# Kernel tuning notes

Measured on AMD Instinct MI355X. Metric: run time of the kernel, lower is better.

Reference implementation:

```python
import jax, jax.numpy as jnp
import numpy as np

T, B, DG, DH, S = 24, 128, 256, 512, 3
LAM, ETA, EPS_A = 0.95, 0.5, 1e-6   # lambda_decay, eta, epsilon (A-update)
LN_EPS = 1e-5                        # torch LayerNorm default eps
EPS_N = 1e-6                         # norm clamp in inner loop


def setup_inputs() -> dict:
    key = jax.random.key(0)
    ks = jax.random.split(key, 3)
    return {
        "z_seq": jax.random.normal(ks[0], (T, B, DG), jnp.float32),
        "W_h": jax.random.normal(ks[1], (DH, DH), jnp.float32) * (2.0 / DH) ** 0.5,  # kaiming-ish
        "W_g": jax.random.normal(ks[2], (DH, DG), jnp.float32) * (1.0 / DG) ** 0.5,  # xavier-ish
        "b_h": jnp.zeros((DH,), jnp.float32),
        "gamma": jnp.ones((DH,), jnp.float32),
        "beta": jnp.zeros((DH,), jnp.float32),
        "alpha_fw": jnp.ones((1,), jnp.float32),
    }


def _layernorm(x, g, b):
    m = jnp.mean(x, -1, keepdims=True)
    v = jnp.mean((x - m) ** 2, -1, keepdims=True)
    return (x - m) * jax.lax.rsqrt(v + LN_EPS) * g + b


def _compute_k(a):
    k_pos = 1.0 + jax.nn.softplus(a)
    k_neg = 1.0 / (1.0 + jax.nn.softplus(-a))
    return jnp.where(a >= 0, k_pos, k_neg)


def reference(z_seq, W_h, W_g, b_h, gamma, beta, alpha_fw):
    k = _compute_k(alpha_fw[0])

    def step(carry, inp):
        h, A = carry            # h: [B, DH], A: [B, DH, DH]
        z_t, upd = inp          # z_t: [B, DG], upd: scalar bool (t < T-1)
        h_base = h @ W_h.T + z_t @ W_g.T + b_h
        h_s = jax.nn.relu(h_base)
        for _ in range(S):      # inner associative-memory iteration
            Ah = jnp.einsum('bij,bj->bi', A, h_s)
            dot = jnp.sum(h_s * Ah, -1, keepdims=True)
            n1 = jnp.maximum(jnp.linalg.norm(h_s, axis=-1, keepdims=True), EPS_N)
            n2 = jnp.maximum(jnp.linalg.norm(Ah, axis=-1, keepdims=True), EPS_N)
            R_pos = jnp.clip(dot / (n1 * n2), 0.0, 1.0)
            alpha_dyn = 1.0 - (1.0 - R_pos) ** k
            h_s = jax.nn.relu(_layernorm((1.0 - alpha_dyn ** 2) * h_base + alpha_dyn * Ah, gamma, beta))
        # fast-weight Hebbian update (skipped at the last timestep)
        hn2 = jnp.sum(h_s ** 2, -1, keepdims=True) + EPS_A            # [B, 1]
        delta = h_s[:, :, None] * h_s[:, None, :] / hn2[:, :, None]   # [B, DH, DH]
        A_new = jnp.where(upd, LAM * A + ETA * delta, A)
        return (h_s, A_new), None

    h0 = jnp.zeros((B, DH), z_seq.dtype)
    A0 = jnp.zeros((B, DH, DH), z_seq.dtype)
    upd = jnp.arange(T) < (T - 1)
    (h, A), _ = jax.lax.scan(step, (h0, A0), (z_seq, upd))
    return h
```

## Files before the change

### kernel.cpp

```cpp
#include <hip/hip_runtime.h>
#include <hip/hip_fp16.h>
#include <math.h>

#define T_STEPS 24
#define BATCH   128
#define DGI     256
#define DHI     512
#define S_ITERS 3
#define LAMBDA  0.95f
#define ETA     0.5f
#define EPS_A   1e-6f
#define LN_EPS  1e-5f
#define EPS_N   1e-6f
#define HIST_MAX 23
#define NG4      6

static __device__ __forceinline__ float dot2(unsigned int a, unsigned int b, float c) {
#if __has_builtin(__builtin_amdgcn_fdot2)
    typedef _Float16 h2v __attribute__((ext_vector_type(2)));
    return __builtin_amdgcn_fdot2(__builtin_bit_cast(h2v, a),
                                  __builtin_bit_cast(h2v, b), c, false);
#else
    const __half2 ha = __builtin_bit_cast(__half2, a);
    const __half2 hb = __builtin_bit_cast(__half2, b);
    const float2 fa = __half22float2(ha);
    const float2 fb = __half22float2(hb);
    return fmaf(fa.x, fb.x, fmaf(fa.y, fb.y, c));
#endif
}

static __device__ __forceinline__ unsigned int rdlane_u(unsigned int v, int l) {
#if __has_builtin(__builtin_amdgcn_readlane)
    return __builtin_amdgcn_readlane(v, l);
#else
    return __shfl((int)v, l, 64);
#endif
}
static __device__ __forceinline__ float rdlane_f(float v, int l) {
    return __uint_as_float(rdlane_u(__float_as_uint(v), l));
}

static __device__ __forceinline__ float wsum(float v) {
    #pragma unroll
    for (int off = 32; off > 0; off >>= 1) v += __shfl_xor(v, off, 64);
    return v;
}
static __device__ __forceinline__ float dot8(float4 a, float4 b, float4 c, float4 d) {
    float r = a.x * c.x;
    r = fmaf(a.y, c.y, r); r = fmaf(a.z, c.z, r); r = fmaf(a.w, c.w, r);
    r = fmaf(b.x, d.x, r); r = fmaf(b.y, d.y, r); r = fmaf(b.z, d.z, r);
    r = fmaf(b.w, d.w, r);
    return r;
}
static __device__ __forceinline__ float sum8(float4 a, float4 b) {
    return ((a.x + a.y) + (a.z + a.w)) + ((b.x + b.y) + (b.z + b.w));
}

__global__ void transpose_k(const float* __restrict__ src, float* __restrict__ dst,
                            int R, int C) {
    __shared__ float tile[32][33];
    const int tx = threadIdx.x & 31;
    const int ty = threadIdx.x >> 5;
    const int c0 = blockIdx.x * 32;
    const int r0 = blockIdx.y * 32;
    #pragma unroll
    for (int i = 0; i < 32; i += 8)
        tile[ty + i][tx] = src[(size_t)(r0 + ty + i) * C + (c0 + tx)];
    __syncthreads();
    #pragma unroll
    for (int i = 0; i < 32; i += 8)
        dst[(size_t)(c0 + ty + i) * R + (r0 + tx)] = tile[tx][ty + i];
}

__global__ __launch_bounds__(512)
void pack_wh_k(const float* __restrict__ Wh, unsigned int* __restrict__ P) {
    const int j2 = blockIdx.x;
    const int i  = threadIdx.x;
    const float2 w = *(const float2*)(Wh + (size_t)i * DHI + 2 * j2);
    const __half2 h = __floats2half2_rn(w.x, w.y);
    P[(size_t)j2 * DHI + i] = __builtin_bit_cast(unsigned int, h);
}

__global__ __launch_bounds__(512)
void zproj_k(const float* __restrict__ z_seq, const float* __restrict__ WgT,
             float* __restrict__ zp) {
    __shared__ __align__(16) float  sh_z[8][DGI];
    __shared__ __align__(16) float4 sh_acc[8][4][128];
    const int b    = blockIdx.x;
    const int t0   = blockIdx.y * 8;
    const int tid  = threadIdx.x;
    const int lane = tid & 63;
    const int wave = tid >> 6;
    {
        const float4* src =
            (const float4*)(z_seq + ((size_t)(t0 + wave) * BATCH + b) * DGI);
        ((float4*)sh_z[wave])[lane] = src[lane];
    }
    __syncthreads();

    const int i4  = tid & 127;
    const int jg  = tid >> 7;
    const int jlo = jg * 64;
    float zreg[8];
    #pragma unroll
    for (int tt = 0; tt < 8; ++tt) zreg[tt] = sh_z[tt][jlo + lane];

    float4 acc[8];
    #pragma unroll
    for (int tt = 0; tt < 8; ++tt) acc[tt] = make_float4(0.f, 0.f, 0.f, 0.f);

    const float4* w4 = (const float4*)WgT;
    #pragma unroll 4
    for (int jj = 0; jj < 64; ++jj) {
        const float4 wv = w4[(size_t)(jlo + jj) * 128 + i4];
        #pragma unroll
        for (int tt = 0; tt < 8; ++tt) {
            const float zv = rdlane_f(zreg[tt], jj);
            acc[tt].x = fmaf(wv.x, zv, acc[tt].x);
            acc[tt].y = fmaf(wv.y, zv, acc[tt].y);
            acc[tt].z = fmaf(wv.z, zv, acc[tt].z);
            acc[tt].w = fmaf(wv.w, zv, acc[tt].w);
        }
    }
    #pragma unroll
    for (int tt = 0; tt < 8; ++tt) sh_acc[tt][jg][i4] = acc[tt];
    __syncthreads();

    const float* af = (const float*)sh_acc;
    #pragma unroll
    for (int tt = 0; tt < 8; ++tt) {
        const int o = tt * 4 * 512;
        const float v = (af[o + tid] + af[o + 512 + tid]) +
                        (af[o + 1024 + tid] + af[o + 1536 + tid]);
        zp[((size_t)b * T_STEPS + t0 + tt) * DHI + tid] = v;
    }
}

__global__ __launch_bounds__(512)
void rnn_v3(const float* __restrict__ zp,
            const unsigned int* __restrict__ P,
            const float* __restrict__ b_h,
            const float* __restrict__ gamma,
            const float* __restrict__ beta,
            const float* __restrict__ alpha_fw,
            float* __restrict__ out) {
    __shared__ __align__(16) float  sh_hist[HIST_MAX][DHI];
    __shared__ __align__(16) float4 sh_hT4[NG4][DHI];
    __shared__ __align__(16) float4 sh_G4[NG4][64];
    __shared__ __align__(16) float  sh_hs[2][DHI];
    __shared__ __align__(16) float  sh_hb[DHI];
    __shared__ __align__(16) float4 sh_part[4][128];
    __shared__ __align__(16) unsigned int sh_h2[DHI / 2];
    __shared__ __align__(16) float  sh_coef[32];
    __shared__ __align__(16) float  sh_dot[32];
    __shared__ __align__(16) float  sh_dhb[32];
    __shared__ __align__(16) float  sh_rsum[32];
    __shared__ float sh_misc[2];

    const int tid  = threadIdx.x;
    const int lane = tid & 63;
    const int wave = tid >> 6;
    const int b    = blockIdx.x;

    const float bh_r = b_h[tid];
    const float g_r  = gamma[tid];
    const float bt_r = beta[tid];

    float kpow;
    {
        const float a  = alpha_fw[0];
        const float ax = fabsf(a);
        const float sp = (ax > 20.f) ? ax : log1pf(expf(ax));
        kpow = (a >= 0.f) ? (1.f + sp) : (1.f / (1.f + sp));
    }

    {
        const float4 z4 = make_float4(0.f, 0.f, 0.f, 0.f);
        for (int i = tid; i < NG4 * DHI; i += DHI) ((float4*)sh_hT4)[i] = z4;
        if (tid < NG4 * 64) ((float4*)sh_G4)[tid] = z4;
        if (tid < 32) { sh_coef[tid] = 0.f; sh_dot[tid] = 0.f;
                        sh_dhb[tid]  = 0.f; sh_rsum[tid] = 0.f; }
        if (tid < 2) sh_misc[tid] = 0.f;
    }
    __syncthreads();

    int   p = 0;
    float hs_i = 0.f, hbase_i = 0.f;
    const size_t zbase = (size_t)b * T_STEPS * DHI + tid;
    float zv = zp[zbase];

    for (int t = 0; t < T_STEPS; ++t) {
        if (t > 0) {
            const int i4 = tid & 127;
            const int jg = tid >> 7;
            const uint4* __restrict__ wp = (const uint4*)P;
            const unsigned int hreg = sh_h2[(jg << 6) | lane];
            const int base = (jg << 6) * 128 + i4;
            float4 acc = make_float4(0.f, 0.f, 0.f, 0.f);
            #pragma unroll 8
            for (int jj = 0; jj < 64; ++jj) {
                const unsigned int hh = rdlane_u(hreg, jj);
                const uint4 wv = wp[base + jj * 128];
                acc.x = dot2(wv.x, hh, acc.x);
                acc.y = dot2(wv.y, hh, acc.y);
                acc.z = dot2(wv.z, hh, acc.z);
                acc.w = dot2(wv.w, hh, acc.w);
            }
            sh_part[jg][i4] = acc;
            __syncthreads();
            const float* pp = (const float*)sh_part;
            hbase_i = bh_r + zv +
                      ((pp[tid] + pp[512 + tid]) + (pp[1024 + tid] + pp[1536 + tid]));
        } else {
            hbase_i = bh_r + zv;
        }
        sh_hb[tid] = hbase_i;
        hs_i = fmaxf(hbase_i, 0.f);
        p ^= 1;
        sh_hs[p][tid] = hs_i;
        __syncthreads();

        if (t + 1 < T_STEPS) zv = zp[zbase + (size_t)(t + 1) * DHI];

        const int niter = (t == 0) ? 1 : S_ITERS;
        for (int it = 0; it < niter; ++it) {
            {
                const float4* h4p = (const float4*)sh_hs[p];
                const float4 ha = h4p[lane], hc = h4p[64 + lane];
                float4 ba, bc;
                if (it == 0) {
                    const float4* b4p = (const float4*)sh_hb;
                    ba = b4p[lane]; bc = b4p[64 + lane];
                }
                for (int s = wave; s <= t; s += 8) {
                    if (s == t) {
                        float d = dot8(ha, hc, ha, hc);
                        if (it == 0) {
                            float s1 = sum8(ba, bc);
                            float s2 = dot8(ba, bc, ba, bc);
                            d = wsum(d); s1 = wsum(s1); s2 = wsum(s2);
                            if (lane == 0) { sh_dot[t] = d;
                                             sh_misc[0] = s1; sh_misc[1] = s2; }
                        } else {
                            d = wsum(d);
                            if (lane == 0) sh_dot[t] = d;
                        }
                    } else {
                        const float4* v4 = (const float4*)sh_hist[s];
                        const float4 va = v4[lane], vc = v4[64 + lane];
                        float d = dot8(va, vc, ha, hc);
                        if (it == 0) {
                            float e = dot8(va, vc, ba, bc);
                            d = wsum(d); e = wsum(e);
                            if (lane == 0) { sh_dot[s] = d; sh_dhb[s] = e; }
                        } else {
                            d = wsum(d);
                            if (lane == 0) sh_dot[s] = d;
                        }
                    }
                }
            }
            __syncthreads();

            float pa = 0.f, SA = 0.f, SHA = 0.f, gsum = 0.f, Ah = 0.f;
            {
                const float4* c4 = (const float4*)sh_coef;
                const float4* d4 = (const float4*)sh_dot;
                const float4* e4 = (const float4*)sh_dhb;
                const float4* r4 = (const float4*)sh_rsum;
                const int ng = (t + 4) >> 2;
                for (int g = 0; g < ng; ++g) {
                    const float4 cc = c4[g], dd = d4[g], ee = e4[g], rr = r4[g];
                    const float4 gg = sh_G4[g][lane];
                    const float4 hv = sh_hT4[g][tid];
                    const float w0 = cc.x * dd.x, w1 = cc.y * dd.y;
                    const float w2 = cc.z * dd.z, w3 = cc.w * dd.w;
                    pa   = fmaf(w0, dd.x, fmaf(w1, dd.y, fmaf(w2, dd.z, fmaf(w3, dd.w, pa))));
                    SA   = fmaf(w0, rr.x, fmaf(w1, rr.y, fmaf(w2, rr.z, fmaf(w3, rr.w, SA))));
                    SHA  = fmaf(w0, ee.x, fmaf(w1, ee.y, fmaf(w2, ee.z, fmaf(w3, ee.w, SHA))));
                    gsum = fmaf(w0, gg.x, fmaf(w1, gg.y, fmaf(w2, gg.z, fmaf(w3, gg.w, gsum))));
                    Ah   = fmaf(w0, hv.x, fmaf(w1, hv.y, fmaf(w2, hv.z, fmaf(w3, hv.w, Ah))));
                }
            }
            const float wl = (lane < 32) ? sh_coef[lane] * sh_dot[lane] : 0.f;
            const float pb = wsum(wl * gsum);

            const float n1 = fmaxf(sqrtf(sh_dot[t]), EPS_N);
            const float n2 = fmaxf(sqrtf(fmaxf(pb, 0.f)), EPS_N);
            float R = pa / (n1 * n2);
            R = fminf(fmaxf(R, 0.f), 1.f);
            const float alpha = 1.f - __powf(1.f - R, kpow);
            const float c = 1.f - alpha * alpha;

            const float S1 = sh_misc[0], S2 = sh_misc[1];
            const float mean = (c * S1 + alpha * SA) * (1.f / DHI);
            float var = (c * c * S2 + 2.f * c * alpha * SHA + alpha * alpha * pb)
                        * (1.f / DHI) - mean * mean;
            var = fmaxf(var, 0.f);
            const float rstd = rsqrtf(var + LN_EPS);

            const float y = fmaf(c, hbase_i, alpha * Ah);
            hs_i = fmaxf(fmaf((y - mean) * rstd, g_r, bt_r), 0.f);
            p ^= 1;
            sh_hs[p][tid] = hs_i;
            if (it == niter - 1 && t + 1 < T_STEPS) {
                const float partner = __shfl_xor(hs_i, 1);
                if (!(tid & 1)) {
                    const __half2 h2 = __floats2half2_rn(hs_i, partner);
                    sh_h2[tid >> 1] = __builtin_bit_cast(unsigned int, h2);
                }
            }
            __syncthreads();
        }

        if (t < T_STEPS - 1) {
            const float4* h4p = (const float4*)sh_hs[p];
            const float4 ha = h4p[lane], hc = h4p[64 + lane];
            for (int s = wave; s <= t; s += 8) {
                if (s == t) {
                    float d  = dot8(ha, hc, ha, hc);
                    float rs = sum8(ha, hc);
                    d = wsum(d); rs = wsum(rs);
                    if (lane == 0) {
                        ((float*)&sh_G4[t >> 2][t])[t & 3] = d;
                        sh_coef[t] = ETA / (d + EPS_A);
                        sh_rsum[t] = rs;
                    }
                } else {
                    const float4* v4 = (const float4*)sh_hist[s];
                    const float4 va = v4[lane], vc = v4[64 + lane];
                    float d = dot8(va, vc, ha, hc);
                    d = wsum(d);
                    if (lane == 0) {
                        ((float*)&sh_G4[t >> 2][s])[t & 3] = d;
                        ((float*)&sh_G4[s >> 2][t])[s & 3] = d;
                    }
                }
            }
            if (tid < t) sh_coef[tid] *= LAMBDA;
            sh_hist[t][tid] = hs_i;
            ((float*)&sh_hT4[t >> 2][tid])[t & 3] = hs_i;
        } else {
            out[(size_t)b * DHI + tid] = hs_i;
        }
    }
}

__global__ __launch_bounds__(512)
void corernn_fb(const float* __restrict__ z_seq, const float* __restrict__ Wh,
                const float* __restrict__ Wg, const float* __restrict__ b_h,
                const float* __restrict__ gamma, const float* __restrict__ beta,
                const float* __restrict__ alpha_fw, float* __restrict__ out) {
    __shared__ __align__(16) float sh_hist[HIST_MAX][DHI];
    __shared__ __align__(16) float sh_hs[2][DHI];
    __shared__ __align__(16) float sh_G[HIST_MAX][64];
    __shared__ float  sh_coef[32];
    __shared__ float  sh_dot[32];
    __shared__ float2 sh_red[8];
    __shared__ __align__(16) float sh_z[DGI];

    const int tid  = threadIdx.x;
    const int lane = tid & 63;
    const int wave = tid >> 6;
    const int b    = blockIdx.x;
    const float bh_r = b_h[tid];
    const float g_r  = gamma[tid];
    const float bt_r = beta[tid];
    float kpow;
    {
        const float a  = alpha_fw[0];
        const float ax = fabsf(a);
        const float sp = (ax > 20.f) ? ax : log1pf(expf(ax));
        kpow = (a >= 0.f) ? (1.f + sp) : (1.f / (1.f + sp));
    }
    for (int i = tid; i < HIST_MAX * 64; i += DHI) ((float*)sh_G)[i] = 0.f;
    if (tid < DGI) sh_z[tid] = z_seq[(size_t)b * DGI + tid];
    __syncthreads();

    int p = 0;
    float hs_i = 0.f, hbase_i = 0.f;
    for (int t = 0; t < T_STEPS; ++t) {
        float a0 = bh_r, a1 = 0.f, a2 = 0.f, a3 = 0.f;
        {
            const float4* wrow = (const float4*)(Wg + (size_t)tid * DGI);
            const float4* z4   = (const float4*)sh_z;
            #pragma unroll 4
            for (int j4 = 0; j4 < DGI / 4; ++j4) {
                const float4 w = wrow[j4]; const float4 h = z4[j4];
                a0 = fmaf(w.x, h.x, a0); a1 = fmaf(w.y, h.y, a1);
                a2 = fmaf(w.z, h.z, a2); a3 = fmaf(w.w, h.w, a3);
            }
        }
        if (t > 0) {
            const float4* wrow = (const float4*)(Wh + (size_t)tid * DHI);
            const float4* h4   = (const float4*)sh_hs[p];
            #pragma unroll 4
            for (int j4 = 0; j4 < DHI / 4; ++j4) {
                const float4 w = wrow[j4]; const float4 h = h4[j4];
                a0 = fmaf(w.x, h.x, a0); a1 = fmaf(w.y, h.y, a1);
                a2 = fmaf(w.z, h.z, a2); a3 = fmaf(w.w, h.w, a3);
            }
        }
        hbase_i = (a0 + a1) + (a2 + a3);
        hs_i = fmaxf(hbase_i, 0.f);
        p ^= 1; sh_hs[p][tid] = hs_i;
        __syncthreads();

        const int niter = (t == 0) ? 1 : S_ITERS;
        for (int it = 0; it < niter; ++it) {
            const float* hcur = sh_hs[p];
            float h8[8];
            #pragma unroll
            for (int q = 0; q < 8; ++q) h8[q] = hcur[lane + 64 * q];
            for (int s = wave; s <= t; s += 8) {
                float d = 0.f;
                if (s == t) {
                    #pragma unroll
                    for (int q = 0; q < 8; ++q) d = fmaf(h8[q], h8[q], d);
                } else {
                    const float* vr = sh_hist[s];
                    #pragma unroll
                    for (int q = 0; q < 8; ++q) d = fmaf(vr[lane + 64 * q], h8[q], d);
                }
                #pragma unroll
                for (int off = 32; off > 0; off >>= 1) d += __shfl_xor(d, off, 64);
                if (lane == 0) sh_dot[s] = d;
            }
            __syncthreads();
            float dl = 0.f, w_l = 0.f;
            if (lane < t) { dl = sh_dot[lane]; w_l = sh_coef[lane] * dl; }
            float gsum = 0.f, Ah = 0.f;
            for (int s = 0; s < t; ++s) {
                const float ws = sh_coef[s] * sh_dot[s];
                gsum = fmaf(ws, sh_G[s][lane], gsum);
                Ah   = fmaf(ws, sh_hist[s][tid], Ah);
            }
            float pa = w_l * dl, pb = w_l * gsum;
            #pragma unroll
            for (int off = 32; off > 0; off >>= 1) {
                pa += __shfl_xor(pa, off, 64);
                pb += __shfl_xor(pb, off, 64);
            }
            const float n1 = fmaxf(sqrtf(sh_dot[t]), EPS_N);
            const float n2 = fmaxf(sqrtf(fmaxf(pb, 0.f)), EPS_N);
            float R = fminf(fmaxf(pa / (n1 * n2), 0.f), 1.f);
            const float alpha = 1.f - __powf(1.f - R, kpow);
            const float y = (1.f - alpha * alpha) * hbase_i + alpha * Ah;
            float q0 = y, q1 = y * y;
            #pragma unroll
            for (int off = 32; off > 0; off >>= 1) {
                q0 += __shfl_xor(q0, off, 64);
                q1 += __shfl_xor(q1, off, 64);
            }
            if (lane == 0) sh_red[wave] = make_float2(q0, q1);
            __syncthreads();
            float s0 = 0.f, s1 = 0.f;
            #pragma unroll
            for (int w = 0; w < 8; ++w) { const float2 r = sh_red[w]; s0 += r.x; s1 += r.y; }
            const float mean = s0 * (1.f / DHI);
            const float var  = fmaf(s1, 1.f / DHI, -mean * mean);
            const float rstd = rsqrtf(var + LN_EPS);
            hs_i = fmaxf(fmaf((y - mean) * rstd, g_r, bt_r), 0.f);
            p ^= 1; sh_hs[p][tid] = hs_i;
            if (it == niter - 1 && t + 1 < T_STEPS && tid < DGI)
                sh_z[tid] = z_seq[((size_t)(t + 1) * BATCH + b) * DGI + tid];
            __syncthreads();
        }

        if (t < T_STEPS - 1) {
            const float* hcur = sh_hs[p];
            float h8[8];
            #pragma unroll
            for (int q = 0; q < 8; ++q) h8[q] = hcur[lane + 64 * q];
            for (int s = wave; s <= t; s += 8) {
                float d = 0.f;
                if (s == t) {
                    #pragma unroll
                    for (int q = 0; q < 8; ++q) d = fmaf(h8[q], h8[q], d);
                } else {
                    const float* vr = sh_hist[s];
                    #pragma unroll
                    for (int q = 0; q < 8; ++q) d = fmaf(vr[lane + 64 * q], h8[q], d);
                }
                #pragma unroll
                for (int off = 32; off > 0; off >>= 1) d += __shfl_xor(d, off, 64);
                if (lane == 0) {
                    if (s == t) { sh_G[t][t] = d; sh_coef[t] = ETA / (d + EPS_A); }
                    else        { sh_G[t][s] = d; sh_G[s][t] = d; }
                }
            }
            if (tid < t) sh_coef[tid] *= LAMBDA;
            sh_hist[t][tid] = hs_i;
        } else {
            out[(size_t)b * DHI + tid] = hs_i;
        }
    }
}

extern "C" void kernel_launch(void* const* d_in, const int* in_sizes, int n_in,
                              void* d_out, int out_size, void* d_ws, size_t ws_size,
                              hipStream_t stream) {
    const float* z_seq    = (const float*)d_in[0];
    const float* W_h      = (const float*)d_in[1];
    const float* W_g      = (const float*)d_in[2];
    const float* b_h      = (const float*)d_in[3];
    const float* gamma    = (const float*)d_in[4];
    const float* beta     = (const float*)d_in[5];
    const float* alpha_fw = (const float*)d_in[6];
    float* out = (float*)d_out;

    const size_t zp_elems  = (size_t)BATCH * T_STEPS * DHI;
    const size_t wgt_elems = (size_t)DGI * DHI;
    const size_t p_elems   = (size_t)(DHI / 2) * DHI;
    const size_t needed = (zp_elems + wgt_elems) * sizeof(float)
                        + p_elems * sizeof(unsigned int);
    if (ws_size >= needed) {
        float* zp  = (float*)d_ws;
        float* WgT = zp + zp_elems;
        unsigned int* P = (unsigned int*)(WgT + wgt_elems);
        transpose_k<<<dim3(DGI / 32, DHI / 32), 256, 0, stream>>>(W_g, WgT, DHI, DGI);
        pack_wh_k<<<DHI / 2, DHI, 0, stream>>>(W_h, P);
        zproj_k<<<dim3(BATCH, T_STEPS / 8), 512, 0, stream>>>(z_seq, WgT, zp);
        rnn_v3<<<BATCH, DHI, 0, stream>>>(zp, P, b_h, gamma, beta, alpha_fw, out);
    } else {
        corernn_fb<<<BATCH, DHI, 0, stream>>>(z_seq, W_h, W_g, b_h, gamma, beta,
                                              alpha_fw, out);
    }
}
```

Measured before the change: 366.3 us.

## Keep half of W_h in registers and double-buffer the rest; merge prep kernels

Before the time loop, each thread now loads 32 uint4 chunks of its packed fp16 W_h slice into registers, so half of the recurrent matvec reads no memory on each step. The other half streams from global memory through a two-slot register double buffer. The W_h pack and W_g transpose kernels are merged into one launch to save a launch. The cost is about 128 extra VGPRs per thread at 512 threads per block, which risks spilling or lower occupancy.

```diff
diff --git a/kernel.cpp b/kernel.cpp
--- a/kernel.cpp
+++ b/kernel.cpp
@@ -56,29 +56,36 @@
     return ((a.x + a.y) + (a.z + a.w)) + ((b.x + b.y) + (b.z + b.w));
 }
 
-__global__ void transpose_k(const float* __restrict__ src, float* __restrict__ dst,
-                            int R, int C) {
+__global__ __launch_bounds__(512)
+void prep_k(const float* __restrict__ Wh, unsigned int* __restrict__ P,
+            const float* __restrict__ Wg, float* __restrict__ WgT) {
     __shared__ float tile[32][33];
-    const int tx = threadIdx.x & 31;
-    const int ty = threadIdx.x >> 5;
-    const int c0 = blockIdx.x * 32;
-    const int r0 = blockIdx.y * 32;
-    #pragma unroll
-    for (int i = 0; i < 32; i += 8)
-        tile[ty + i][tx] = src[(size_t)(r0 + ty + i) * C + (c0 + tx)];
-    __syncthreads();
-    #pragma unroll
-    for (int i = 0; i < 32; i += 8)
-        dst[(size_t)(c0 + ty + i) * R + (r0 + tx)] = tile[tx][ty + i];
-}
-
-__global__ __launch_bounds__(512)
-void pack_wh_k(const float* __restrict__ Wh, unsigned int* __restrict__ P) {
-    const int j2 = blockIdx.x;
-    const int i  = threadIdx.x;
-    const float2 w = *(const float2*)(Wh + (size_t)i * DHI + 2 * j2);
-    const __half2 h = __floats2half2_rn(w.x, w.y);
-    P[(size_t)j2 * DHI + i] = __builtin_bit_cast(unsigned int, h);
+    const int blk = blockIdx.x;
+    if (blk < 256) {
+        const int j2 = blk;
+        const int i  = threadIdx.x;
+        const float2 w = *(const float2*)(Wh + (size_t)i * DHI + 2 * j2);
+        const __half2 h = __floats2half2_rn(w.x, w.y);
+        P[(size_t)j2 * DHI + i] = __builtin_bit_cast(unsigned int, h);
+    } else {
+        const int tb = blk - 256;
+        const int c0 = (tb & 7) * 32;
+        const int r0 = (tb >> 3) * 32;
+        const int tx = threadIdx.x & 31;
+        const int ty = (threadIdx.x >> 5) & 7;
+        const bool act = threadIdx.x < 256;
+        if (act) {
+            #pragma unroll
+            for (int i = 0; i < 32; i += 8)
+                tile[ty + i][tx] = Wg[(size_t)(r0 + ty + i) * DGI + (c0 + tx)];
+        }
+        __syncthreads();
+        if (act) {
+            #pragma unroll
+            for (int i = 0; i < 32; i += 8)
+                WgT[(size_t)(c0 + ty + i) * DHI + (r0 + tx)] = tile[tx][ty + i];
+        }
+    }
 }
 
 __global__ __launch_bounds__(512)
@@ -137,7 +144,7 @@
 }
 
 __global__ __launch_bounds__(512)
-void rnn_v3(const float* __restrict__ zp,
+void rnn_v4(const float* __restrict__ zp,
             const unsigned int* __restrict__ P,
             const float* __restrict__ b_h,
             const float* __restrict__ gamma,
@@ -174,6 +181,14 @@
         kpow = (a >= 0.f) ? (1.f + sp) : (1.f / (1.f + sp));
     }
 
+    const int i4  = tid & 127;
+    const int jg  = tid >> 7;
+    const uint4* __restrict__ wp = (const uint4*)P;
+    const int wbase = (jg << 6) * 128 + i4;
+    uint4 Wpre[32];
+    #pragma unroll
+    for (int k = 0; k < 32; ++k) Wpre[k] = wp[wbase + k * 128];
+
     {
         const float4 z4 = make_float4(0.f, 0.f, 0.f, 0.f);
         for (int i = tid; i < NG4 * DHI; i += DHI) ((float4*)sh_hT4)[i] = z4;
@@ -191,20 +206,37 @@
 
     for (int t = 0; t < T_STEPS; ++t) {
         if (t > 0) {
-            const int i4 = tid & 127;
-            const int jg = tid >> 7;
-            const uint4* __restrict__ wp = (const uint4*)P;
             const unsigned int hreg = sh_h2[(jg << 6) | lane];
-            const int base = (jg << 6) * 128 + i4;
             float4 acc = make_float4(0.f, 0.f, 0.f, 0.f);
-            #pragma unroll 8
-            for (int jj = 0; jj < 64; ++jj) {
+            uint4 cbuf[2][4];
+            #pragma unroll
+            for (int k = 0; k < 4; ++k) cbuf[0][k] = wp[wbase + (32 + k) * 128];
+            #pragma unroll
+            for (int jj = 0; jj < 32; ++jj) {
                 const unsigned int hh = rdlane_u(hreg, jj);
-                const uint4 wv = wp[base + jj * 128];
+                const uint4 wv = Wpre[jj];
                 acc.x = dot2(wv.x, hh, acc.x);
                 acc.y = dot2(wv.y, hh, acc.y);
                 acc.z = dot2(wv.z, hh, acc.z);
                 acc.w = dot2(wv.w, hh, acc.w);
+            }
+            #pragma unroll
+            for (int ch = 0; ch < 8; ++ch) {
+                if (ch < 7) {
+                    #pragma unroll
+                    for (int k = 0; k < 4; ++k)
+                        cbuf[(ch + 1) & 1][k] = wp[wbase + (36 + ch * 4 + k) * 128];
+                }
+                #pragma unroll
+                for (int k = 0; k < 4; ++k) {
+                    const int jj = 32 + ch * 4 + k;
+                    const unsigned int hh = rdlane_u(hreg, jj);
+                    const uint4 wv = cbuf[ch & 1][k];
+                    acc.x = dot2(wv.x, hh, acc.x);
+                    acc.y = dot2(wv.y, hh, acc.y);
+                    acc.z = dot2(wv.z, hh, acc.z);
+                    acc.w = dot2(wv.w, hh, acc.w);
+                }
             }
             sh_part[jg][i4] = acc;
             __syncthreads();
@@ -518,12 +550,11 @@
         float* zp  = (float*)d_ws;
         float* WgT = zp + zp_elems;
         unsigned int* P = (unsigned int*)(WgT + wgt_elems);
-        transpose_k<<<dim3(DGI / 32, DHI / 32), 256, 0, stream>>>(W_g, WgT, DHI, DGI);
-        pack_wh_k<<<DHI / 2, DHI, 0, stream>>>(W_h, P);
+        prep_k<<<384, 512, 0, stream>>>(W_h, P, W_g, WgT);
         zproj_k<<<dim3(BATCH, T_STEPS / 8), 512, 0, stream>>>(z_seq, WgT, zp);
-        rnn_v3<<<BATCH, DHI, 0, stream>>>(zp, P, b_h, gamma, beta, alpha_fw, out);
+        rnn_v4<<<BATCH, 512, 0, stream>>>(zp, P, b_h, gamma, beta, alpha_fw, out);
     } else {
-        corernn_fb<<<BATCH, DHI, 0, stream>>>(z_seq, W_h, W_g, b_h, gamma, beta,
+        corernn_fb<<<BATCH, 512, 0, stream>>>(z_seq, W_h, W_g, b_h, gamma, beta,
                                               alpha_fw, out);
     }
 }
```

Measured after the change: 378.5 us. +3.4%, slower.
